# Optimization experiments

Hardware: AMD Instinct MI355X
Metric: run time of the kernel (lower is better)

The kernel has to match this reference:

```python
import jax, jax.numpy as jnp
import numpy as np

N_SUB = 262144      # total subgraphs (rows of h_subgraph)
NUM_GRAPHS = 8192   # graphs in batch
D = 128             # channel width
L = 3               # number of fc / fc_sum layers
NUM_TASKS = 10


def segment_mean(x, idx, num_segments):
    # scatter_mean: sum per segment, divide by count (count>=1 guard like torch_scatter)
    sums = jax.ops.segment_sum(x, idx, num_segments=num_segments)
    cnt = jax.ops.segment_sum(jnp.ones((x.shape[0],), dtype=x.dtype), idx, num_segments=num_segments)
    return sums / jnp.maximum(cnt, 1.0)[:, None]


def setup_inputs() -> dict:
    key = jax.random.key(0)
    ks = jax.random.split(key, 10)
    s = 1.0 / np.sqrt(D)
    h_subgraph = jax.random.normal(ks[0], (N_SUB, D), dtype=jnp.float32)
    subgraph_idx = jnp.sort(jax.random.randint(ks[1], (N_SUB,), 0, NUM_GRAPHS, dtype=jnp.int32))
    W_fc = jax.random.normal(ks[2], (L, D, D), dtype=jnp.float32) * s
    b_fc = jax.random.normal(ks[3], (L, D), dtype=jnp.float32) * s
    W_sum = jax.random.normal(ks[4], (L, D, D), dtype=jnp.float32) * s
    b_sum = jax.random.normal(ks[5], (L, D), dtype=jnp.float32) * s
    W_f1 = jax.random.normal(ks[6], (D, 2 * D), dtype=jnp.float32) * s
    b_f1 = jax.random.normal(ks[7], (2 * D,), dtype=jnp.float32) * s
    W_f2 = jax.random.normal(ks[8], (2 * D, NUM_TASKS), dtype=jnp.float32) / np.sqrt(2 * D)
    b_f2 = jax.random.normal(ks[9], (NUM_TASKS,), dtype=jnp.float32) / np.sqrt(2 * D)
    return {"h_subgraph": h_subgraph, "subgraph_idx": subgraph_idx,
            "W_fc": W_fc, "b_fc": b_fc, "W_sum": W_sum, "b_sum": b_sum,
            "W_f1": W_f1, "b_f1": b_f1, "W_f2": W_f2, "b_f2": b_f2}


def reference(h_subgraph, subgraph_idx, W_fc, b_fc, W_sum, b_sum, W_f1, b_f1, W_f2, b_f2):
    h = h_subgraph
    # non-invariant branch: per-layer Linear + scatter_mean + Linear + gather + ELU
    for i in range(L):
        x1 = h @ W_fc[i] + b_fc[i]                                  # [N, D]
        g = segment_mean(h, subgraph_idx, NUM_GRAPHS)               # [G, D]
        x2 = g @ W_sum[i] + b_sum[i]                                # [G, D]
        h = jax.nn.elu(x1 + x2[subgraph_idx])                       # gather + combine
    h_graph = segment_mean(h, subgraph_idx, NUM_GRAPHS)             # [G, D]
    # final MLP head
    out = jax.nn.relu(h_graph @ W_f1 + b_f1) @ W_f2 + b_f2          # [G, num_tasks]
    return out
```

## Files before the change

### kernel.cpp

```cpp
#include <hip/hip_runtime.h>

#define NSUB 262144
#define NG   8192
#define DIM  128
#define NT   10

typedef __attribute__((ext_vector_type(4))) float f32x4;
typedef __attribute__((ext_vector_type(8))) short short8;
typedef unsigned short ushort_t;
typedef unsigned int uint_t;

__device__ __forceinline__ float bf2f(ushort_t u){
    union { uint_t i; float f; } v; v.i = ((uint_t)u) << 16; return v.f;
}
__device__ __forceinline__ ushort_t f2bf(float f){
    union { __bf16 b; ushort_t u; } v; v.b = (__bf16)f; return v.u;
}


__global__ __launch_bounds__(256) void prep_kernel(const float* __restrict__ Wfc,
                                                   ushort_t* __restrict__ Wt,
                                                   float* __restrict__ g,
                                                   float* __restrict__ cnt)
{
    const int b = blockIdx.x;
    if (b < 2056){
        const long t = (long)b * 256 + threadIdx.x;
        const f32x4 z = {0.f, 0.f, 0.f, 0.f};
        if (t < 524288) ((f32x4*)g)[t] = z;
        else            ((f32x4*)cnt)[t - 524288] = z;
    } else {
        int t = (b - 2056) * 256 + threadIdx.x;
        int i   = t >> 11;
        int rem = t & 2047;
        int ks  = rem >> 9;
        int f   = (rem >> 6) & 7;
        int l   = rem & 63;
        int c   = f * 16 + (l & 15);
        int kb  = ks * 32 + (l >> 4) * 8;
        short8 v;
        #pragma unroll
        for (int j = 0; j < 8; j++)
            v[j] = (short)f2bf(Wfc[i * 16384 + (kb + j) * 128 + c]);
        *(short8*)(Wt + (long)t * 8) = v;
    }
}

__global__ __launch_bounds__(256) void conv0_kernel(const float* __restrict__ h0,
                                                    const int* __restrict__ idx,
                                                    ushort_t* __restrict__ hfrag,
                                                    float* __restrict__ gsum,
                                                    float* __restrict__ cnt)
{
    __shared__ int sidx[128];
    __shared__ __align__(16) char fb[128 * 272];
    const int tid = threadIdx.x;
    const int bid = ((blockIdx.x & 7) << 8) | (blockIdx.x >> 3);
    const long base = (long)bid * 128;
    if (tid < 128) sidx[tid] = idx[base + tid];

    const int cg = tid & 31, ch = tid >> 5;
    const int rloc0 = ch * 16;

    f32x4 v[16];
    #pragma unroll
    for (int j = 0; j < 16; j++)
        v[j] = *(const f32x4*)(h0 + (base + rloc0 + j) * 128 + cg * 4);
    #pragma unroll
    for (int j = 0; j < 16; j++){
        uint2 pk;
        pk.x = (uint_t)f2bf(v[j][0]) | ((uint_t)f2bf(v[j][1]) << 16);
        pk.y = (uint_t)f2bf(v[j][2]) | ((uint_t)f2bf(v[j][3]) << 16);
        *(uint2*)(fb + (rloc0 + j) * 272 + cg * 8) = pk;
    }
    __syncthreads();

    {
        const int r15 = tid & 15, grp = (tid >> 4) & 3, ks = tid >> 6;
        f32x4* dst = (f32x4*)hfrag + (long)bid * 2048 + tid;
        const char* srcrow = fb + ks * 64 + grp * 16;
        #pragma unroll
        for (int rg = 0; rg < 8; rg++){
            f32x4 val = *(const f32x4*)(srcrow + (rg * 16 + r15) * 272);
            dst[rg * 256] = val;
        }
    }

    f32x4 acc = {0.f, 0.f, 0.f, 0.f};
    int cur = sidx[rloc0], n = 0;
    #pragma unroll
    for (int j = 0; j < 16; j++){
        const int g = sidx[rloc0 + j];
        if (g != cur){
            float* gp = gsum + (long)cur * 128 + cg * 4;
            atomicAdd(gp + 0, acc[0]); atomicAdd(gp + 1, acc[1]);
            atomicAdd(gp + 2, acc[2]); atomicAdd(gp + 3, acc[3]);
            if (cg == 0) atomicAdd(cnt + cur, (float)n);
            acc = {0.f, 0.f, 0.f, 0.f}; n = 0; cur = g;
        }
        acc += v[j]; n++;
    }
    float* gp = gsum + (long)cur * 128 + cg * 4;
    atomicAdd(gp + 0, acc[0]); atomicAdd(gp + 1, acc[1]);
    atomicAdd(gp + 2, acc[2]); atomicAdd(gp + 3, acc[3]);
    if (cg == 0) atomicAdd(cnt + cur, (float)n);
}

__global__ __launch_bounds__(256) void x2_kernel(float* g,
                                                 const float* __restrict__ cnt,
                                                 const float* __restrict__ Wsum,
                                                 const float* __restrict__ bsum,
                                                 const float* __restrict__ bfc,
                                                 float* __restrict__ x2)
{
    __shared__ float gm[16][128];
    __shared__ float invc[16];
    const int tid = threadIdx.x;
    const int r0 = blockIdx.x * 16;
    if (tid < 16) invc[tid] = 1.f / fmaxf(cnt[r0 + tid], 1.f);
    __syncthreads();
    #pragma unroll
    for (int p = 0; p < 8; p++){
        int e = tid + p * 256;
        int row = e >> 7, col = e & 127;
        float val = g[(long)(r0 + row) * 128 + col];
        gm[row][col] = val * invc[row];
        g[(long)(r0 + row) * 128 + col] = 0.f;
    }
    __syncthreads();
    const int c = tid & 127, rh = tid >> 7;
    float acc[8];
    #pragma unroll
    for (int i = 0; i < 8; i++) acc[i] = bsum[c] + bfc[c];
    for (int k = 0; k < 128; k++){
        float w = Wsum[k * 128 + c];
        #pragma unroll
        for (int i = 0; i < 8; i++) acc[i] += gm[rh * 8 + i][k] * w;
    }
    #pragma unroll
    for (int i = 0; i < 8; i++) x2[(long)(r0 + rh * 8 + i) * 128 + c] = acc[i];
}

__global__ __launch_bounds__(256, 4) void layer_kernel(ushort_t* hbuf,
                                                    const ushort_t* __restrict__ Wt,
                                                    const float* __restrict__ x2,
                                                    const int* __restrict__ idx,
                                                    float* __restrict__ gnext)
{
    __shared__ __align__(16) ushort_t seg[128 * 132];
    __shared__ int sidx[128];
    const int tid = threadIdx.x;
    const int bid = ((blockIdx.x & 7) << 8) | (blockIdx.x >> 3);
    const long base = (long)bid * 128;

    const int wv = tid >> 6, ln = tid & 63;
    const int ln15 = ln & 15, grp = ln >> 4;
    const long Rbase = (long)bid * 8 + wv * 2;

    short8 b8[8];
    #pragma unroll
    for (int ks = 0; ks < 4; ks++)
        #pragma unroll
        for (int q = 0; q < 2; q++)
            b8[ks * 2 + q] = *(const short8*)(hbuf + (((Rbase + q) * 4 + ks) * 64 + ln) * 8);

    if (tid < 128) sidx[tid] = idx[base + tid];

    f32x4 acc[2][8];
    #pragma unroll
    for (int q = 0; q < 2; q++)
        #pragma unroll
        for (int f = 0; f < 8; f++) acc[q][f] = {0.f, 0.f, 0.f, 0.f};

    __builtin_amdgcn_s_setprio(1);
    #pragma unroll
    for (int ks = 0; ks < 4; ks++){
        short8 a0[4], a1[4];
        #pragma unroll
        for (int f = 0; f < 4; f++)
            a0[f] = *(const short8*)(Wt + ((long)(ks * 8 + f) * 64 + ln) * 8);
        #pragma unroll
        for (int f = 0; f < 4; f++)
            #pragma unroll
            for (int q = 0; q < 2; q++)
                acc[q][f] = __builtin_amdgcn_mfma_f32_16x16x32_bf16(a0[f], b8[ks * 2 + q], acc[q][f], 0, 0, 0);
        #pragma unroll
        for (int f = 0; f < 4; f++)
            a1[f] = *(const short8*)(Wt + ((long)(ks * 8 + 4 + f) * 64 + ln) * 8);
        #pragma unroll
        for (int f = 0; f < 4; f++)
            #pragma unroll
            for (int q = 0; q < 2; q++)
                acc[q][4 + f] = __builtin_amdgcn_mfma_f32_16x16x32_bf16(a1[f], b8[ks * 2 + q], acc[q][4 + f], 0, 0, 0);
    }
    __builtin_amdgcn_s_setprio(0);

    #pragma unroll
    for (int q = 0; q < 2; q++){
        const int lr = wv * 32 + q * 16 + ln15;
        const int g = idx[base + lr];
        const float* x2r = x2 + (long)g * 128;
        f32x4 xv[8];
        #pragma unroll
        for (int f = 0; f < 8; f++)
            xv[f] = *(const f32x4*)(x2r + f * 16 + grp * 4);
        #pragma unroll
        for (int f = 0; f < 8; f++){
            const int cb = f * 16 + grp * 4;
            ushort_t h4[4];
            #pragma unroll
            for (int i = 0; i < 4; i++){
                float v = acc[q][f][i] + xv[f][i];
                v = v > 0.f ? v : (__expf(v) - 1.f);
                h4[i] = f2bf(v);
            }
            uint2 pk;
            pk.x = (uint_t)h4[0] | ((uint_t)h4[1] << 16);
            pk.y = (uint_t)h4[2] | ((uint_t)h4[3] << 16);
            const long c16 = ((Rbase + q) * 4 + (f >> 1)) * 64
                           + (2 * (f & 1) + (grp >> 1)) * 16 + ln15;
            *(uint2*)((char*)hbuf + c16 * 16 + (grp & 1) * 8) = pk;
            *(uint2*)((char*)seg + lr * 264 + cb * 2) = pk;
        }
    }
    __syncthreads();

    const int c = tid & 63, ch2 = tid >> 6;
    const int rr0 = ch2 * 32;
    float a0 = 0.f, a1 = 0.f;
    int cur = sidx[rr0];
    for (int j = 0; j < 32; j++){
        const int rr = rr0 + j;
        const int g = sidx[rr];
        if (g != cur){
            atomicAdd(gnext + (long)cur * 128 + 2 * c,     a0);
            atomicAdd(gnext + (long)cur * 128 + 2 * c + 1, a1);
            a0 = a1 = 0.f; cur = g;
        }
        uint_t u = *(const uint_t*)((const char*)seg + rr * 264 + c * 4);
        a0 += bf2f((ushort_t)(u & 0xffff));
        a1 += bf2f((ushort_t)(u >> 16));
    }
    atomicAdd(gnext + (long)cur * 128 + 2 * c,     a0);
    atomicAdd(gnext + (long)cur * 128 + 2 * c + 1, a1);
}

__global__ __launch_bounds__(256) void head_kernel(const float* __restrict__ g,
                                                   const float* __restrict__ cnt,
                                                   const float* __restrict__ Wf1,
                                                   const float* __restrict__ bf1,
                                                   const float* __restrict__ Wf2,
                                                   const float* __restrict__ bf2,
                                                   float* __restrict__ out)
{
    __shared__ float hm[8][128];
    __shared__ float t1[8][256];
    __shared__ float invc[8];
    const int tid = threadIdx.x;
    const int r0 = blockIdx.x * 8;
    if (tid < 8) invc[tid] = 1.f / fmaxf(cnt[r0 + tid], 1.f);
    __syncthreads();
    #pragma unroll
    for (int p = 0; p < 4; p++){
        int e = tid + p * 256;
        int row = e >> 7, col = e & 127;
        hm[row][col] = g[(long)(r0 + row) * 128 + col] * invc[row];
    }
    __syncthreads();
    {
        const int c = tid;
        float acc[8];
        #pragma unroll
        for (int r = 0; r < 8; r++) acc[r] = bf1[c];
        for (int k = 0; k < 128; k++){
            float w = Wf1[k * 256 + c];
            #pragma unroll
            for (int r = 0; r < 8; r++) acc[r] += hm[r][k] * w;
        }
        #pragma unroll
        for (int r = 0; r < 8; r++) t1[r][c] = fmaxf(acc[r], 0.f);
    }
    __syncthreads();
    if (tid < 80){
        const int r = tid / 10, c = tid % 10;
        float acc = bf2[c];
        for (int k = 0; k < 256; k++) acc += t1[r][k] * Wf2[k * 10 + c];
        out[(long)(r0 + r) * 10 + c] = acc;
    }
}

extern "C" void kernel_launch(void* const* d_in, const int* in_sizes, int n_in,
                              void* d_out, int out_size, void* d_ws, size_t ws_size,
                              hipStream_t stream)
{
    const float* h0   = (const float*)d_in[0];
    const int*   idx  = (const int*)d_in[1];
    const float* Wfc  = (const float*)d_in[2];
    const float* bfc  = (const float*)d_in[3];
    const float* Wsum = (const float*)d_in[4];
    const float* bsum = (const float*)d_in[5];
    const float* Wf1  = (const float*)d_in[6];
    const float* bf1  = (const float*)d_in[7];
    const float* Wf2  = (const float*)d_in[8];
    const float* bf2  = (const float*)d_in[9];
    float* out = (float*)d_out;

    char* ws = (char*)d_ws;
    ushort_t* hbuf = (ushort_t*)ws;
    float* g0  = (float*)(ws + 67108864);
    float* g1  = (float*)(ws + 71303168);
    float* x2  = (float*)(ws + 75497472);
    float* cnt = (float*)(ws + 79691776);
    ushort_t* Wt = (ushort_t*)(ws + 79724544);
    if (ws_size < 79822848ull) return;

    prep_kernel<<<2080, 256, 0, stream>>>(Wfc, Wt, g0, cnt);

    conv0_kernel<<<NSUB / 128, 256, 0, stream>>>(h0, idx, hbuf, g0, cnt);
    x2_kernel<<<NG / 16, 256, 0, stream>>>(g0, cnt, Wsum, bsum, bfc, x2);
    layer_kernel<<<NSUB / 128, 256, 0, stream>>>(hbuf, Wt, x2, idx, g1);

    x2_kernel<<<NG / 16, 256, 0, stream>>>(g1, cnt, Wsum + 16384, bsum + 128, bfc + 128, x2);
    layer_kernel<<<NSUB / 128, 256, 0, stream>>>(hbuf, Wt + 16384, x2, idx, g0);

    x2_kernel<<<NG / 16, 256, 0, stream>>>(g0, cnt, Wsum + 32768, bsum + 256, bfc + 256, x2);
    layer_kernel<<<NSUB / 128, 256, 0, stream>>>(hbuf, Wt + 32768, x2, idx, g1);

    head_kernel<<<NG / 8, 256, 0, stream>>>(g1, cnt, Wf1, bf1, Wf2, bf2, out);
}
```

Before: 239.6 us.

## Drop bf16 staging pass; first layer reads fp32 input directly

Replaces the conv0 kernel, which converted the fp32 input to bf16 fragments and wrote them out, with a plain segment-sum kernel. The first layer kernel is templated so it loads fp32 rows directly and converts them to bf16 MFMA fragments in registers. This removes a full write and read-back of the bf16 copy, at the cost of reading the fp32 input twice and using less contiguous fp32 loads in the layer kernel.

```diff
diff --git a/kernel.cpp b/kernel.cpp
--- a/kernel.cpp
+++ b/kernel.cpp
@@ -46,46 +46,20 @@
     }
 }
 
-__global__ __launch_bounds__(256) void conv0_kernel(const float* __restrict__ h0,
-                                                    const int* __restrict__ idx,
-                                                    ushort_t* __restrict__ hfrag,
-                                                    float* __restrict__ gsum,
-                                                    float* __restrict__ cnt)
+__global__ __launch_bounds__(256) void seg0_kernel(const float* __restrict__ h0,
+                                                   const int* __restrict__ idx,
+                                                   float* __restrict__ gsum,
+                                                   float* __restrict__ cnt)
 {
     __shared__ int sidx[128];
-    __shared__ __align__(16) char fb[128 * 272];
     const int tid = threadIdx.x;
     const int bid = ((blockIdx.x & 7) << 8) | (blockIdx.x >> 3);
     const long base = (long)bid * 128;
     if (tid < 128) sidx[tid] = idx[base + tid];
+    __syncthreads();
 
     const int cg = tid & 31, ch = tid >> 5;
     const int rloc0 = ch * 16;
-
-    f32x4 v[16];
-    #pragma unroll
-    for (int j = 0; j < 16; j++)
-        v[j] = *(const f32x4*)(h0 + (base + rloc0 + j) * 128 + cg * 4);
-    #pragma unroll
-    for (int j = 0; j < 16; j++){
-        uint2 pk;
-        pk.x = (uint_t)f2bf(v[j][0]) | ((uint_t)f2bf(v[j][1]) << 16);
-        pk.y = (uint_t)f2bf(v[j][2]) | ((uint_t)f2bf(v[j][3]) << 16);
-        *(uint2*)(fb + (rloc0 + j) * 272 + cg * 8) = pk;
-    }
-    __syncthreads();
-
-    {
-        const int r15 = tid & 15, grp = (tid >> 4) & 3, ks = tid >> 6;
-        f32x4* dst = (f32x4*)hfrag + (long)bid * 2048 + tid;
-        const char* srcrow = fb + ks * 64 + grp * 16;
-        #pragma unroll
-        for (int rg = 0; rg < 8; rg++){
-            f32x4 val = *(const f32x4*)(srcrow + (rg * 16 + r15) * 272);
-            dst[rg * 256] = val;
-        }
-    }
-
     f32x4 acc = {0.f, 0.f, 0.f, 0.f};
     int cur = sidx[rloc0], n = 0;
     #pragma unroll
@@ -98,7 +72,8 @@
             if (cg == 0) atomicAdd(cnt + cur, (float)n);
             acc = {0.f, 0.f, 0.f, 0.f}; n = 0; cur = g;
         }
-        acc += v[j]; n++;
+        f32x4 v = *(const f32x4*)(h0 + (base + rloc0 + j) * 128 + cg * 4);
+        acc += v; n++;
     }
     float* gp = gsum + (long)cur * 128 + cg * 4;
     atomicAdd(gp + 0, acc[0]); atomicAdd(gp + 1, acc[1]);
@@ -141,7 +116,9 @@
     for (int i = 0; i < 8; i++) x2[(long)(r0 + rh * 8 + i) * 128 + c] = acc[i];
 }
 
-__global__ __launch_bounds__(256, 4) void layer_kernel(ushort_t* hbuf,
+template<int FIRST>
+__global__ __launch_bounds__(256, 4) void layer_kernel(const void* __restrict__ hin_,
+                                                    ushort_t* hout,
                                                     const ushort_t* __restrict__ Wt,
                                                     const float* __restrict__ x2,
                                                     const int* __restrict__ idx,
@@ -158,11 +135,36 @@
     const long Rbase = (long)bid * 8 + wv * 2;
 
     short8 b8[8];
-    #pragma unroll
-    for (int ks = 0; ks < 4; ks++)
-        #pragma unroll
-        for (int q = 0; q < 2; q++)
-            b8[ks * 2 + q] = *(const short8*)(hbuf + (((Rbase + q) * 4 + ks) * 64 + ln) * 8);
+    if (FIRST){
+        const float* hp = (const float*)hin_;
+        f32x4 hv[16];
+        #pragma unroll
+        for (int ks = 0; ks < 4; ks++)
+            #pragma unroll
+            for (int q = 0; q < 2; q++){
+                const long r = (Rbase + q) * 16 + ln15;
+                const float* p = hp + r * 128 + ks * 32 + grp * 8;
+                hv[(ks * 2 + q) * 2 + 0] = *(const f32x4*)p;
+                hv[(ks * 2 + q) * 2 + 1] = *(const f32x4*)(p + 4);
+            }
+        #pragma unroll
+        for (int i = 0; i < 8; i++){
+            short8 s;
+            #pragma unroll
+            for (int j = 0; j < 4; j++){
+                s[j]     = (short)f2bf(hv[2 * i][j]);
+                s[4 + j] = (short)f2bf(hv[2 * i + 1][j]);
+            }
+            b8[i] = s;
+        }
+    } else {
+        const ushort_t* hp = (const ushort_t*)hin_;
+        #pragma unroll
+        for (int ks = 0; ks < 4; ks++)
+            #pragma unroll
+            for (int q = 0; q < 2; q++)
+                b8[ks * 2 + q] = *(const short8*)(hp + (((Rbase + q) * 4 + ks) * 64 + ln) * 8);
+    }
 
     if (tid < 128) sidx[tid] = idx[base + tid];
 
@@ -219,7 +221,7 @@
             pk.y = (uint_t)h4[2] | ((uint_t)h4[3] << 16);
             const long c16 = ((Rbase + q) * 4 + (f >> 1)) * 64
                            + (2 * (f & 1) + (grp >> 1)) * 16 + ln15;
-            *(uint2*)((char*)hbuf + c16 * 16 + (grp & 1) * 8) = pk;
+            *(uint2*)((char*)hout + c16 * 16 + (grp & 1) * 8) = pk;
             *(uint2*)((char*)seg + lr * 264 + cb * 2) = pk;
         }
     }
@@ -316,15 +318,15 @@
 
     prep_kernel<<<2080, 256, 0, stream>>>(Wfc, Wt, g0, cnt);
 
-    conv0_kernel<<<NSUB / 128, 256, 0, stream>>>(h0, idx, hbuf, g0, cnt);
+    seg0_kernel<<<NSUB / 128, 256, 0, stream>>>(h0, idx, g0, cnt);
     x2_kernel<<<NG / 16, 256, 0, stream>>>(g0, cnt, Wsum, bsum, bfc, x2);
-    layer_kernel<<<NSUB / 128, 256, 0, stream>>>(hbuf, Wt, x2, idx, g1);
+    layer_kernel<1><<<NSUB / 128, 256, 0, stream>>>(h0, hbuf, Wt, x2, idx, g1);
 
     x2_kernel<<<NG / 16, 256, 0, stream>>>(g1, cnt, Wsum + 16384, bsum + 128, bfc + 128, x2);
-    layer_kernel<<<NSUB / 128, 256, 0, stream>>>(hbuf, Wt + 16384, x2, idx, g0);
+    layer_kernel<0><<<NSUB / 128, 256, 0, stream>>>(hbuf, hbuf, Wt + 16384, x2, idx, g0);
 
     x2_kernel<<<NG / 16, 256, 0, stream>>>(g0, cnt, Wsum + 32768, bsum + 256, bfc + 256, x2);
-    layer_kernel<<<NSUB / 128, 256, 0, stream>>>(hbuf, Wt + 32768, x2, idx, g1);
+    layer_kernel<0><<<NSUB / 128, 256, 0, stream>>>(hbuf, hbuf, Wt + 32768, x2, idx, g1);
 
     head_kernel<<<NG / 8, 256, 0, stream>>>(g1, cnt, Wf1, bf1, Wf2, bf2, out);
 }
```

Result: slower. 245.5 us (+2.5%).
